# Optimization experiments

Measured on AMD Instinct MI355X. Metric: run time of the kernel, lower is better.

## Reference

```python
import jax, jax.numpy as jnp
import numpy as np

VOCAB = 4096
HIDDEN = 1024
BATCH = 64
SEQ = 256


def setup_inputs() -> dict:
    key = jax.random.key(0)
    ks = jax.random.split(key, 9)
    s = 0.02
    D = VOCAB + HIDDEN
    return {
        "X": jax.random.randint(ks[0], (BATCH, SEQ), 0, VOCAB),
        # gate weights stored as [in, out] = [VOCAB+HIDDEN, HIDDEN] (transposed torch Linear)
        "Wz": jax.random.normal(ks[1], (D, HIDDEN), dtype=jnp.float32) * s,
        "bz": jax.random.normal(ks[2], (HIDDEN,), dtype=jnp.float32) * s,
        "Wr": jax.random.normal(ks[3], (D, HIDDEN), dtype=jnp.float32) * s,
        "br": jax.random.normal(ks[4], (HIDDEN,), dtype=jnp.float32) * s,
        "Wh": jax.random.normal(ks[5], (D, HIDDEN), dtype=jnp.float32) * s,
        "bh": jax.random.normal(ks[6], (HIDDEN,), dtype=jnp.float32) * s,
        "Wo": jax.random.normal(ks[7], (HIDDEN, VOCAB), dtype=jnp.float32) * s,
        "bo": jax.random.normal(ks[8], (VOCAB,), dtype=jnp.float32) * s,
    }


def reference(X, Wz, bz, Wr, br, Wh, bh, Wo, bo):
    # X: [B, S] int tokens. torch does one_hot(X.T) -> time-major [S, B, V].
    # one_hot @ W_input_block == row gather of the input block of each gate weight.
    Xt = X.T  # [S, B]
    Wz_x, Wz_h = Wz[:VOCAB], Wz[VOCAB:]
    Wr_x, Wr_h = Wr[:VOCAB], Wr[VOCAB:]
    Wh_x, Wh_h = Wh[:VOCAB], Wh[VOCAB:]

    H0 = jnp.zeros((X.shape[0], HIDDEN), dtype=Wz.dtype)

    def step(H, x_t):
        # x_t: [B] int
        z = jax.nn.sigmoid(Wz_x[x_t] + H @ Wz_h + bz)
        r = jax.nn.sigmoid(Wr_x[x_t] + H @ Wr_h + br)
        h = jnp.tanh(Wh_x[x_t] + (r * H) @ Wh_h + bh)
        H_new = z * h + (1.0 - z) * H
        Y = H_new @ Wo + bo  # [B, V]
        return H_new, Y

    H_final, Ys = jax.lax.scan(step, H0, Xt)  # Ys: [S, B, V]
    # torch.cat(outputs, dim=0) over S tensors of [B, V] -> [S*B, V]
    out = Ys.reshape(-1, VOCAB)
    return out, (H_final,)
```

## Files before the change

### kernel.cpp

```cpp
#include <hip/hip_runtime.h>
#include <hip/hip_bf16.h>
#include <cstdint>
#include <cstddef>

#define VOCAB  4096
#define HIDDEN 1024
#define BATCH  64
#define SEQ    256
#define NWG    64

typedef __attribute__((ext_vector_type(8))) short short8;
typedef __attribute__((ext_vector_type(4))) float f32x4;
typedef unsigned long long u64;

__device__ __forceinline__ unsigned short f2bf(float f) {
    union { float f; uint32_t u; } v; v.f = f;
    uint32_t u = v.u;
    u += 0x7FFFu + ((u >> 16) & 1u);
    return (unsigned short)(u >> 16);
}

__device__ __forceinline__ void ast16(unsigned short* p, unsigned short v) {
    __hip_atomic_store(p, v, __ATOMIC_RELAXED, __HIP_MEMORY_SCOPE_AGENT);
}

__device__ __forceinline__ short8 cld16(const unsigned short* p) {
    short8 v;
    asm volatile("global_load_dwordx4 %0, %1, off sc0 sc1"
                 : "=v"(v) : "v"(p) : "memory");
    return v;
}

__global__ __launch_bounds__(256) void k_zero(float* Hf, unsigned short* Hbf, int* flags) {
    int i = blockIdx.x * 256 + threadIdx.x;
    if (i < BATCH * HIDDEN) { Hf[i] = 0.f; Hbf[i] = 0; }
    if (i < NWG * 32) flags[i] = 0;
}

__global__ __launch_bounds__(256) void k_pack(const float* __restrict__ src,
                                              unsigned short* __restrict__ dst,
                                              int R, int C) {
    __shared__ float tile[32][33];
    int tilesC = C >> 5;
    int bx = blockIdx.x % tilesC;
    int by = blockIdx.x / tilesC;
    int tx = threadIdx.x & 31;
    int ty = threadIdx.x >> 5;
    int c0 = bx << 5, r0 = by << 5;
    #pragma unroll
    for (int s = 0; s < 4; ++s) {
        int r = ty + s * 8;
        tile[r][tx] = src[(size_t)(r0 + r) * C + (c0 + tx)];
    }
    __syncthreads();
    #pragma unroll
    for (int s = 0; s < 4; ++s) {
        int cc = ty + s * 8;
        dst[(size_t)(c0 + cc) * R + (r0 + tx)] = f2bf(tile[tx][cc]);
    }
}

__device__ __forceinline__ void flag_barrier(int* flags, int p) {
    __syncthreads();
    if (threadIdx.x == 0)
        __hip_atomic_store(&flags[blockIdx.x * 32], p, __ATOMIC_RELEASE, __HIP_MEMORY_SCOPE_AGENT);
    if (threadIdx.x < NWG) {
        while (__hip_atomic_load(&flags[threadIdx.x * 32], __ATOMIC_RELAXED, __HIP_MEMORY_SCOPE_AGENT) < p)
            __builtin_amdgcn_s_sleep(1);
    }
    __syncthreads();
}

__global__ __launch_bounds__(256, 1) void k_scan(
    const int* __restrict__ X,
    const float* __restrict__ Wz, const float* __restrict__ bz,
    const float* __restrict__ Wr, const float* __restrict__ br,
    const float* __restrict__ Wh, const float* __restrict__ bh,
    const unsigned short* __restrict__ Wzh, const unsigned short* __restrict__ Wrh,
    const unsigned short* __restrict__ Whh,
    float* __restrict__ Hf, unsigned short* __restrict__ Hbf,
    unsigned short* __restrict__ rHbf, unsigned short* __restrict__ Hhist,
    int* __restrict__ flags)
{
    __shared__ __align__(16) unsigned short WzL[16 * 1024];
    __shared__ __align__(16) unsigned short WrL[16 * 1024];
    __shared__ __align__(16) unsigned short WhL[16 * 1024];

    const int tid  = threadIdx.x;
    const int g    = blockIdx.x;
    const int w    = tid >> 6;
    const int lane = tid & 63;
    const int row  = lane & 15;
    const int q    = lane >> 4;
    const int kq   = q << 3;
    const int col0 = g << 4;
    const int j    = col0 + row;
    const int b0   = w << 4;
    const int bq   = b0 + (q << 2);

    #pragma unroll
    for (int c = 0; c < 8; ++c) {
        int idx = tid + c * 256;
        int kkg = idx >> 6;
        int rem = idx & 63;
        int qq  = rem >> 4;
        int rr  = rem & 15;
        size_t srcoff = (size_t)(col0 + rr) * HIDDEN + kkg * 32 + qq * 8;
        *(short8*)&WzL[idx * 8] = *(const short8*)&Wzh[srcoff];
        *(short8*)&WrL[idx * 8] = *(const short8*)&Wrh[srcoff];
        *(short8*)&WhL[idx * 8] = *(const short8*)&Whh[srcoff];
    }
    __syncthreads();

    const float bzj = bz[j], brj = br[j], bhj = bh[j];

    float zreg[4] = {0.f, 0.f, 0.f, 0.f};
    float Hreg[4] = {0.f, 0.f, 0.f, 0.f};
    int p = 0;

    int   tok[4];
    float ez[4], er[4], eh[4];
    #pragma unroll
    for (int r = 0; r < 4; ++r) {
        tok[r] = X[(bq + r) * SEQ + 0];
        ez[r]  = Wz[(size_t)tok[r] * HIDDEN + j];
        er[r]  = Wr[(size_t)tok[r] * HIDDEN + j];
        eh[r]  = Wh[(size_t)tok[r] * HIDDEN + j];
    }

    for (int t = 0; t < SEQ; ++t) {
        {
            const unsigned short* ap = Hbf + (size_t)(b0 + row) * HIDDEN + kq;
            short8 A[32];
            #pragma unroll
            for (int kk = 0; kk < 32; ++kk)
                A[kk] = cld16(ap + kk * 32);

            f32x4 accZ = {0.f, 0.f, 0.f, 0.f}, accR = {0.f, 0.f, 0.f, 0.f};
            asm volatile("s_waitcnt vmcnt(16)" ::: "memory");
            __builtin_amdgcn_sched_barrier(0);
            #pragma unroll
            for (int kk = 0; kk < 16; ++kk) {
                short8 bzf = *(const short8*)&WzL[kk * 512 + q * 128 + row * 8];
                short8 brf = *(const short8*)&WrL[kk * 512 + q * 128 + row * 8];
                accZ = __builtin_amdgcn_mfma_f32_16x16x32_bf16(A[kk], bzf, accZ, 0, 0, 0);
                accR = __builtin_amdgcn_mfma_f32_16x16x32_bf16(A[kk], brf, accR, 0, 0, 0);
            }
            asm volatile("s_waitcnt vmcnt(0)" ::: "memory");
            __builtin_amdgcn_sched_barrier(0);
            #pragma unroll
            for (int kk = 16; kk < 32; ++kk) {
                short8 bzf = *(const short8*)&WzL[kk * 512 + q * 128 + row * 8];
                short8 brf = *(const short8*)&WrL[kk * 512 + q * 128 + row * 8];
                accZ = __builtin_amdgcn_mfma_f32_16x16x32_bf16(A[kk], bzf, accZ, 0, 0, 0);
                accR = __builtin_amdgcn_mfma_f32_16x16x32_bf16(A[kk], brf, accR, 0, 0, 0);
            }
            #pragma unroll
            for (int r = 0; r < 4; ++r) {
                float rr = 1.f / (1.f + expf(-(accR[r] + er[r] + brj)));
                ast16(&rHbf[(bq + r) * HIDDEN + j], f2bf(rr * Hreg[r]));
            }
            #pragma unroll
            for (int r = 0; r < 4; ++r)
                zreg[r] = 1.f / (1.f + expf(-(accZ[r] + ez[r] + bzj)));
        }

        flag_barrier(flags, ++p);

        {
            const unsigned short* ap = rHbf + (size_t)(b0 + row) * HIDDEN + kq;
            short8 A[32];
            #pragma unroll
            for (int kk = 0; kk < 32; ++kk)
                A[kk] = cld16(ap + kk * 32);

            f32x4 accA = {0.f, 0.f, 0.f, 0.f}, accB = {0.f, 0.f, 0.f, 0.f};
            asm volatile("s_waitcnt vmcnt(16)" ::: "memory");
            __builtin_amdgcn_sched_barrier(0);
            #pragma unroll
            for (int kk = 0; kk < 16; ++kk) {
                short8 bf = *(const short8*)&WhL[kk * 512 + q * 128 + row * 8];
                if (kk & 1) accB = __builtin_amdgcn_mfma_f32_16x16x32_bf16(A[kk], bf, accB, 0, 0, 0);
                else        accA = __builtin_amdgcn_mfma_f32_16x16x32_bf16(A[kk], bf, accA, 0, 0, 0);
            }
            asm volatile("s_waitcnt vmcnt(0)" ::: "memory");
            __builtin_amdgcn_sched_barrier(0);
            #pragma unroll
            for (int kk = 16; kk < 32; ++kk) {
                short8 bf = *(const short8*)&WhL[kk * 512 + q * 128 + row * 8];
                if (kk & 1) accB = __builtin_amdgcn_mfma_f32_16x16x32_bf16(A[kk], bf, accB, 0, 0, 0);
                else        accA = __builtin_amdgcn_mfma_f32_16x16x32_bf16(A[kk], bf, accA, 0, 0, 0);
            }
            #pragma unroll
            for (int r = 0; r < 4; ++r) {
                int b = bq + r;
                float h  = tanhf(accA[r] + accB[r] + eh[r] + bhj);
                float Hn = zreg[r] * h + (1.f - zreg[r]) * Hreg[r];
                Hreg[r] = Hn;
                unsigned short bfv = f2bf(Hn);
                ast16(&Hbf[b * HIDDEN + j], bfv);
                Hhist[(size_t)t * (BATCH * HIDDEN) + b * HIDDEN + j] = bfv;
                if (t == SEQ - 1) Hf[b * HIDDEN + j] = Hn;
            }
        }

        if (t + 1 < SEQ) {
            #pragma unroll
            for (int r = 0; r < 4; ++r) {
                tok[r] = X[(bq + r) * SEQ + (t + 1)];
                ez[r]  = Wz[(size_t)tok[r] * HIDDEN + j];
                er[r]  = Wr[(size_t)tok[r] * HIDDEN + j];
                eh[r]  = Wh[(size_t)tok[r] * HIDDEN + j];
            }
        }

        flag_barrier(flags, ++p);
    }
}

__global__ __launch_bounds__(256) void k_step1(
    const int* __restrict__ X,
    const float* __restrict__ Wz, const float* __restrict__ bz,
    const float* __restrict__ Wr, const float* __restrict__ br,
    const unsigned short* __restrict__ Wzh, const unsigned short* __restrict__ Wrh,
    const unsigned short* __restrict__ Hbf, const float* __restrict__ Hf,
    float* __restrict__ zbuf, unsigned short* __restrict__ rHbf, int t)
{
    int w    = threadIdx.x >> 6;
    int lane = threadIdx.x & 63;
    int nt = blockIdx.x;
    int mt = w;
    bool isz = nt < 64;
    const unsigned short* W = isz ? Wzh : Wrh;
    int ntl = nt & 63;
    int row = lane & 15;
    int kq  = (lane >> 4) << 3;
    const unsigned short* aptr = Hbf + (size_t)(mt * 16 + row) * HIDDEN + kq;
    const unsigned short* bptr = W   + (size_t)(ntl * 16 + row) * HIDDEN + kq;
    f32x4 acc = {0.f, 0.f, 0.f, 0.f};
    #pragma unroll 8
    for (int kk = 0; kk < HIDDEN / 32; ++kk) {
        short8 a = *(const short8*)(aptr + kk * 32);
        short8 b = *(const short8*)(bptr + kk * 32);
        acc = __builtin_amdgcn_mfma_f32_16x16x32_bf16(a, b, acc, 0, 0, 0);
    }
    int j = ntl * 16 + row;
    const float* Wemb = isz ? Wz : Wr;
    float bias = isz ? bz[j] : br[j];
    #pragma unroll
    for (int r = 0; r < 4; ++r) {
        int b = mt * 16 + ((lane >> 4) << 2) + r;
        int tok = X[b * SEQ + t];
        float pre = acc[r] + Wemb[(size_t)tok * HIDDEN + j] + bias;
        float s = 1.f / (1.f + expf(-pre));
        if (isz) zbuf[b * HIDDEN + j] = s;
        else     rHbf[b * HIDDEN + j] = f2bf(s * Hf[b * HIDDEN + j]);
    }
}

__global__ __launch_bounds__(256) void k_step2(
    const int* __restrict__ X,
    const float* __restrict__ Wh, const float* __restrict__ bh,
    const unsigned short* __restrict__ Whh,
    const unsigned short* __restrict__ rHbf,
    const float* __restrict__ zbuf,
    float* __restrict__ Hf, unsigned short* __restrict__ Hbf,
    unsigned short* __restrict__ Hhist, int t)
{
    int w    = threadIdx.x >> 6;
    int lane = threadIdx.x & 63;
    int nt = blockIdx.x;
    int mt = w;
    int row = lane & 15;
    int kq  = (lane >> 4) << 3;
    const unsigned short* aptr = rHbf + (size_t)(mt * 16 + row) * HIDDEN + kq;
    const unsigned short* bptr = Whh  + (size_t)(nt * 16 + row) * HIDDEN + kq;
    f32x4 acc = {0.f, 0.f, 0.f, 0.f};
    #pragma unroll 8
    for (int kk = 0; kk < HIDDEN / 32; ++kk) {
        short8 a = *(const short8*)(aptr + kk * 32);
        short8 b = *(const short8*)(bptr + kk * 32);
        acc = __builtin_amdgcn_mfma_f32_16x16x32_bf16(a, b, acc, 0, 0, 0);
    }
    int j = nt * 16 + row;
    float bias = bh[j];
    #pragma unroll
    for (int r = 0; r < 4; ++r) {
        int b = mt * 16 + ((lane >> 4) << 2) + r;
        int tok = X[b * SEQ + t];
        float pre = acc[r] + Wh[(size_t)tok * HIDDEN + j] + bias;
        float h = tanhf(pre);
        float z = zbuf[b * HIDDEN + j];
        float Hold = Hf[b * HIDDEN + j];
        float Hn = z * h + (1.f - z) * Hold;
        Hf[b * HIDDEN + j] = Hn;
        unsigned short bf = f2bf(Hn);
        Hbf[b * HIDDEN + j] = bf;
        Hhist[(size_t)t * (BATCH * HIDDEN) + b * HIDDEN + j] = bf;
    }
}

__global__ __launch_bounds__(256) void k_out(
    const unsigned short* __restrict__ A,
    const unsigned short* __restrict__ B,
    const float* __restrict__ bo,
    float* __restrict__ out)
{
    __shared__ __align__(16) unsigned short As[128 * 32];
    __shared__ __align__(16) unsigned short Bs[128 * 32];
    int bn = blockIdx.x & 31;
    int bm = blockIdx.x >> 5;
    int m0 = bm << 7, n0 = bn << 7;
    int tid  = threadIdx.x;
    int w    = tid >> 6, lane = tid & 63;
    int wm = w & 1, wn = w >> 1;
    int row = lane & 15;
    int kq  = (lane >> 4) << 3;

    f32x4 acc[4][4];
    #pragma unroll
    for (int i = 0; i < 4; ++i)
        #pragma unroll
        for (int jj = 0; jj < 4; ++jj)
            acc[i][jj] = (f32x4){0.f, 0.f, 0.f, 0.f};

    for (int k0 = 0; k0 < HIDDEN; k0 += 32) {
        #pragma unroll
        for (int c = 0; c < 2; ++c) {
            int off  = tid * 32 + c * 16;
            int rowi = off >> 6;
            int us   = (off & 63) >> 1;
            *(short8*)&As[rowi * 32 + us] =
                *(const short8*)&A[(size_t)(m0 + rowi) * HIDDEN + k0 + us];
            *(short8*)&Bs[rowi * 32 + us] =
                *(const short8*)&B[(size_t)(n0 + rowi) * HIDDEN + k0 + us];
        }
        __syncthreads();
        short8 a[4], b[4];
        #pragma unroll
        for (int i = 0; i < 4; ++i)
            a[i] = *(const short8*)&As[(wm * 64 + i * 16 + row) * 32 + kq];
        #pragma unroll
        for (int jj = 0; jj < 4; ++jj)
            b[jj] = *(const short8*)&Bs[(wn * 64 + jj * 16 + row) * 32 + kq];
        #pragma unroll
        for (int i = 0; i < 4; ++i)
            #pragma unroll
            for (int jj = 0; jj < 4; ++jj)
                acc[i][jj] = __builtin_amdgcn_mfma_f32_16x16x32_bf16(a[i], b[jj], acc[i][jj], 0, 0, 0);
        __syncthreads();
    }

    #pragma unroll
    for (int i = 0; i < 4; ++i) {
        #pragma unroll
        for (int jj = 0; jj < 4; ++jj) {
            int n = n0 + wn * 64 + jj * 16 + row;
            float bb = bo[n];
            #pragma unroll
            for (int r = 0; r < 4; ++r) {
                int m = m0 + wm * 64 + i * 16 + ((lane >> 4) << 2) + r;
                out[(size_t)m * VOCAB + n] = acc[i][jj][r] + bb;
            }
        }
    }
}

__global__ __launch_bounds__(256) void k_copyH(const float* __restrict__ Hf,
                                               float* __restrict__ out) {
    int i = blockIdx.x * 256 + threadIdx.x;
    if (i < BATCH * HIDDEN)
        out[(size_t)SEQ * BATCH * VOCAB + i] = Hf[i];
}

extern "C" void kernel_launch(void* const* d_in, const int* in_sizes, int n_in,
                              void* d_out, int out_size, void* d_ws, size_t ws_size,
                              hipStream_t stream) {
    const int*   X  = (const int*)  d_in[0];
    const float* Wz = (const float*)d_in[1];
    const float* bz = (const float*)d_in[2];
    const float* Wr = (const float*)d_in[3];
    const float* br = (const float*)d_in[4];
    const float* Wh = (const float*)d_in[5];
    const float* bh = (const float*)d_in[6];
    const float* Wo = (const float*)d_in[7];
    const float* bo = (const float*)d_in[8];
    float* out = (float*)d_out;
    char* ws = (char*)d_ws;

    float*          Hf    = (float*)(ws);
    float*          zbuf  = (float*)(ws + (256 << 10));
    int*            flags = (int*)(ws + (512 << 10));
    unsigned short* Hbf   = (unsigned short*)(ws + (528 << 10));
    unsigned short* rHbf  = (unsigned short*)(ws + (656 << 10));
    unsigned short* Wzh   = (unsigned short*)(ws + (1 << 20));
    unsigned short* Wrh   = Wzh + 1024 * 1024;
    unsigned short* Whh   = Wrh + 1024 * 1024;
    unsigned short* WoT   = Whh + 1024 * 1024;
    unsigned short* Hhist = WoT + (size_t)VOCAB * HIDDEN;

    k_zero<<<256, 256, 0, stream>>>(Hf, Hbf, flags);
    k_pack<<<32 * 32,  256, 0, stream>>>(Wz + (size_t)VOCAB * HIDDEN, Wzh, 1024, 1024);
    k_pack<<<32 * 32,  256, 0, stream>>>(Wr + (size_t)VOCAB * HIDDEN, Wrh, 1024, 1024);
    k_pack<<<32 * 32,  256, 0, stream>>>(Wh + (size_t)VOCAB * HIDDEN, Whh, 1024, 1024);
    k_pack<<<32 * 128, 256, 0, stream>>>(Wo, WoT, 1024, 4096);

    void* args[] = {
        (void*)&X, (void*)&Wz, (void*)&bz, (void*)&Wr, (void*)&br,
        (void*)&Wh, (void*)&bh, (void*)&Wzh, (void*)&Wrh, (void*)&Whh,
        (void*)&Hf, (void*)&Hbf, (void*)&rHbf, (void*)&Hhist, (void*)&flags
    };
    hipError_t cerr = hipLaunchCooperativeKernel((void*)k_scan, dim3(NWG), dim3(256),
                                                 args, 0, stream);
    if (cerr != hipSuccess) {
        for (int t = 0; t < SEQ; ++t) {
            k_step1<<<128, 256, 0, stream>>>(X, Wz, bz, Wr, br, Wzh, Wrh, Hbf, Hf, zbuf, rHbf, t);
            k_step2<<<64,  256, 0, stream>>>(X, Wh, bh, Whh, rHbf, zbuf, Hf, Hbf, Hhist, t);
        }
    }

    k_out<<<4096, 256, 0, stream>>>(Hhist, WoT, bo, out);
    k_copyH<<<256, 256, 0, stream>>>(Hf, out);
}
```

Before: 3.810 ms.

## Split scan into four independent batch groups with 16-workgroup barriers

Reorganizes the persistent scan kernel so each group of 16 workgroups handles 16 batch rows over all hidden columns, rather than every workgroup covering all 64 batch rows for 16 columns. The cross-workgroup barrier now synchronizes only the 16 workgroups of one group instead of all 64. The hidden-state tile is staged once per step into swizzled LDS, and the recurrent weights are streamed from global/L2 each step instead of being held resident in LDS. The intent is cheaper synchronization, at the cost of re-reading the weights every step and more global traffic.

```diff
diff --git a/kernel.cpp b/kernel.cpp
--- a/kernel.cpp
+++ b/kernel.cpp
@@ -8,10 +8,10 @@
 #define BATCH  64
 #define SEQ    256
 #define NWG    64
+#define SCANS  4
 
 typedef __attribute__((ext_vector_type(8))) short short8;
 typedef __attribute__((ext_vector_type(4))) float f32x4;
-typedef unsigned long long u64;
 
 __device__ __forceinline__ unsigned short f2bf(float f) {
     union { float f; uint32_t u; } v; v.f = f;
@@ -34,7 +34,7 @@
 __global__ __launch_bounds__(256) void k_zero(float* Hf, unsigned short* Hbf, int* flags) {
     int i = blockIdx.x * 256 + threadIdx.x;
     if (i < BATCH * HIDDEN) { Hf[i] = 0.f; Hbf[i] = 0; }
-    if (i < NWG * 32) flags[i] = 0;
+    if (i < 2048) flags[i] = 0;
 }
 
 __global__ __launch_bounds__(256) void k_pack(const float* __restrict__ src,
@@ -60,15 +60,18 @@
     }
 }
 
-__device__ __forceinline__ void flag_barrier(int* flags, int p) {
+__device__ __forceinline__ void grp_barrier(int* flags, int base, int idx, int p) {
+    asm volatile("s_waitcnt vmcnt(0)" ::: "memory");
     __syncthreads();
     if (threadIdx.x == 0)
-        __hip_atomic_store(&flags[blockIdx.x * 32], p, __ATOMIC_RELEASE, __HIP_MEMORY_SCOPE_AGENT);
-    if (threadIdx.x < NWG) {
-        while (__hip_atomic_load(&flags[threadIdx.x * 32], __ATOMIC_RELAXED, __HIP_MEMORY_SCOPE_AGENT) < p)
+        __hip_atomic_store(&flags[base + idx], p, __ATOMIC_RELAXED, __HIP_MEMORY_SCOPE_AGENT);
+    if (threadIdx.x < 16) {
+        while (__hip_atomic_load(&flags[base + (int)threadIdx.x],
+                                 __ATOMIC_RELAXED, __HIP_MEMORY_SCOPE_AGENT) < p)
             __builtin_amdgcn_s_sleep(1);
     }
     __syncthreads();
+    __builtin_amdgcn_sched_barrier(0);
 }
 
 __global__ __launch_bounds__(256, 1) void k_scan(
@@ -82,119 +85,124 @@
     unsigned short* __restrict__ rHbf, unsigned short* __restrict__ Hhist,
     int* __restrict__ flags)
 {
-    __shared__ __align__(16) unsigned short WzL[16 * 1024];
-    __shared__ __align__(16) unsigned short WrL[16 * 1024];
-    __shared__ __align__(16) unsigned short WhL[16 * 1024];
+    __shared__ __align__(16) unsigned short ALD[16 * 1024];
 
     const int tid  = threadIdx.x;
     const int g    = blockIdx.x;
-    const int w    = tid >> 6;
+    const int scan = g >> 4;
+    const int wgc  = g & 15;
+    const int wv   = tid >> 6;
     const int lane = tid & 63;
     const int row  = lane & 15;
     const int q    = lane >> 4;
     const int kq   = q << 3;
-    const int col0 = g << 4;
-    const int j    = col0 + row;
-    const int b0   = w << 4;
+    const int j    = (wgc << 6) + (wv << 4) + row;
+    const int b0   = scan << 4;
     const int bq   = b0 + (q << 2);
-
-    #pragma unroll
-    for (int c = 0; c < 8; ++c) {
-        int idx = tid + c * 256;
-        int kkg = idx >> 6;
-        int rem = idx & 63;
-        int qq  = rem >> 4;
-        int rr  = rem & 15;
-        size_t srcoff = (size_t)(col0 + rr) * HIDDEN + kkg * 32 + qq * 8;
-        *(short8*)&WzL[idx * 8] = *(const short8*)&Wzh[srcoff];
-        *(short8*)&WrL[idx * 8] = *(const short8*)&Wrh[srcoff];
-        *(short8*)&WhL[idx * 8] = *(const short8*)&Whh[srcoff];
-    }
-    __syncthreads();
+    const int fbase = scan << 4;
 
     const float bzj = bz[j], brj = br[j], bhj = bh[j];
+    const unsigned short* wzp = Wzh + (size_t)j * HIDDEN + kq;
+    const unsigned short* wrp = Wrh + (size_t)j * HIDDEN + kq;
+    const unsigned short* whp = Whh + (size_t)j * HIDDEN + kq;
 
     float zreg[4] = {0.f, 0.f, 0.f, 0.f};
     float Hreg[4] = {0.f, 0.f, 0.f, 0.f};
     int p = 0;
 
-    int   tok[4];
-    float ez[4], er[4], eh[4];
-    #pragma unroll
-    for (int r = 0; r < 4; ++r) {
-        tok[r] = X[(bq + r) * SEQ + 0];
-        ez[r]  = Wz[(size_t)tok[r] * HIDDEN + j];
-        er[r]  = Wr[(size_t)tok[r] * HIDDEN + j];
-        eh[r]  = Wh[(size_t)tok[r] * HIDDEN + j];
-    }
+    int tokc[4];
+    #pragma unroll
+    for (int r = 0; r < 4; ++r) tokc[r] = X[(bq + r) * SEQ + 0];
 
     for (int t = 0; t < SEQ; ++t) {
+        const int tn = (t + 1 < SEQ) ? t + 1 : t;
+        int tokn[4];
+
         {
-            const unsigned short* ap = Hbf + (size_t)(b0 + row) * HIDDEN + kq;
-            short8 A[32];
-            #pragma unroll
-            for (int kk = 0; kk < 32; ++kk)
-                A[kk] = cld16(ap + kk * 32);
+            {
+                short8 tmp[8];
+                #pragma unroll
+                for (int c = 0; c < 8; ++c) {
+                    int ch = (tid << 3) + c;
+                    int rw = ch >> 7;
+                    int k8 = ch & 127;
+                    tmp[c] = cld16(Hbf + (size_t)(b0 + rw) * HIDDEN + (k8 << 3));
+                }
+                asm volatile("s_waitcnt vmcnt(0)" ::: "memory");
+                __builtin_amdgcn_sched_barrier(0);
+                #pragma unroll
+                for (int c = 0; c < 8; ++c) {
+                    int ch = (tid << 3) + c;
+                    int rw = ch >> 7;
+                    int k8 = ch & 127;
+                    int ui = ((rw << 10) + (k8 << 3)) ^ ((rw & 7) << 3);
+                    *(short8*)&ALD[ui] = tmp[c];
+                }
+                __syncthreads();
+            }
+
+            float ez[4], er[4], eh[4];
+            #pragma unroll
+            for (int r = 0; r < 4; ++r) {
+                size_t eo = (size_t)tokc[r] * HIDDEN + j;
+                ez[r] = Wz[eo]; er[r] = Wr[eo]; eh[r] = Wh[eo];
+                tokn[r] = X[(bq + r) * SEQ + tn];
+            }
 
             f32x4 accZ = {0.f, 0.f, 0.f, 0.f}, accR = {0.f, 0.f, 0.f, 0.f};
-            asm volatile("s_waitcnt vmcnt(16)" ::: "memory");
-            __builtin_amdgcn_sched_barrier(0);
-            #pragma unroll
-            for (int kk = 0; kk < 16; ++kk) {
-                short8 bzf = *(const short8*)&WzL[kk * 512 + q * 128 + row * 8];
-                short8 brf = *(const short8*)&WrL[kk * 512 + q * 128 + row * 8];
-                accZ = __builtin_amdgcn_mfma_f32_16x16x32_bf16(A[kk], bzf, accZ, 0, 0, 0);
-                accR = __builtin_amdgcn_mfma_f32_16x16x32_bf16(A[kk], brf, accR, 0, 0, 0);
-            }
-            asm volatile("s_waitcnt vmcnt(0)" ::: "memory");
-            __builtin_amdgcn_sched_barrier(0);
-            #pragma unroll
-            for (int kk = 16; kk < 32; ++kk) {
-                short8 bzf = *(const short8*)&WzL[kk * 512 + q * 128 + row * 8];
-                short8 brf = *(const short8*)&WrL[kk * 512 + q * 128 + row * 8];
-                accZ = __builtin_amdgcn_mfma_f32_16x16x32_bf16(A[kk], bzf, accZ, 0, 0, 0);
-                accR = __builtin_amdgcn_mfma_f32_16x16x32_bf16(A[kk], brf, accR, 0, 0, 0);
+            #pragma unroll 8
+            for (int kk = 0; kk < 32; ++kk) {
+                int ai = ((row << 10) + (kk << 5) + kq) ^ ((row & 7) << 3);
+                short8 a  = *(const short8*)&ALD[ai];
+                short8 fz = *(const short8*)(wzp + kk * 32);
+                short8 fr = *(const short8*)(wrp + kk * 32);
+                accZ = __builtin_amdgcn_mfma_f32_16x16x32_bf16(a, fz, accZ, 0, 0, 0);
+                accR = __builtin_amdgcn_mfma_f32_16x16x32_bf16(a, fr, accR, 0, 0, 0);
             }
             #pragma unroll
             for (int r = 0; r < 4; ++r) {
-                float rr = 1.f / (1.f + expf(-(accR[r] + er[r] + brj)));
-                ast16(&rHbf[(bq + r) * HIDDEN + j], f2bf(rr * Hreg[r]));
-            }
-            #pragma unroll
-            for (int r = 0; r < 4; ++r)
+                float rv = 1.f / (1.f + expf(-(accR[r] + er[r] + brj)));
+                ast16(&rHbf[(bq + r) * HIDDEN + j], f2bf(rv * Hreg[r]));
                 zreg[r] = 1.f / (1.f + expf(-(accZ[r] + ez[r] + bzj)));
-        }
-
-        flag_barrier(flags, ++p);
-
-        {
-            const unsigned short* ap = rHbf + (size_t)(b0 + row) * HIDDEN + kq;
-            short8 A[32];
-            #pragma unroll
-            for (int kk = 0; kk < 32; ++kk)
-                A[kk] = cld16(ap + kk * 32);
-
-            f32x4 accA = {0.f, 0.f, 0.f, 0.f}, accB = {0.f, 0.f, 0.f, 0.f};
-            asm volatile("s_waitcnt vmcnt(16)" ::: "memory");
-            __builtin_amdgcn_sched_barrier(0);
-            #pragma unroll
-            for (int kk = 0; kk < 16; ++kk) {
-                short8 bf = *(const short8*)&WhL[kk * 512 + q * 128 + row * 8];
-                if (kk & 1) accB = __builtin_amdgcn_mfma_f32_16x16x32_bf16(A[kk], bf, accB, 0, 0, 0);
-                else        accA = __builtin_amdgcn_mfma_f32_16x16x32_bf16(A[kk], bf, accA, 0, 0, 0);
-            }
-            asm volatile("s_waitcnt vmcnt(0)" ::: "memory");
-            __builtin_amdgcn_sched_barrier(0);
-            #pragma unroll
-            for (int kk = 16; kk < 32; ++kk) {
-                short8 bf = *(const short8*)&WhL[kk * 512 + q * 128 + row * 8];
-                if (kk & 1) accB = __builtin_amdgcn_mfma_f32_16x16x32_bf16(A[kk], bf, accB, 0, 0, 0);
-                else        accA = __builtin_amdgcn_mfma_f32_16x16x32_bf16(A[kk], bf, accA, 0, 0, 0);
+            }
+            #pragma unroll
+            for (int r = 0; r < 4; ++r) zreg[r] = zreg[r];
+            grp_barrier(flags, fbase, wgc, ++p);
+
+            {
+                short8 tmp[8];
+                #pragma unroll
+                for (int c = 0; c < 8; ++c) {
+                    int ch = (tid << 3) + c;
+                    int rw = ch >> 7;
+                    int k8 = ch & 127;
+                    tmp[c] = cld16(rHbf + (size_t)(b0 + rw) * HIDDEN + (k8 << 3));
+                }
+                asm volatile("s_waitcnt vmcnt(0)" ::: "memory");
+                __builtin_amdgcn_sched_barrier(0);
+                #pragma unroll
+                for (int c = 0; c < 8; ++c) {
+                    int ch = (tid << 3) + c;
+                    int rw = ch >> 7;
+                    int k8 = ch & 127;
+                    int ui = ((rw << 10) + (k8 << 3)) ^ ((rw & 7) << 3);
+                    *(short8*)&ALD[ui] = tmp[c];
+                }
+                __syncthreads();
+            }
+
+            f32x4 accH = {0.f, 0.f, 0.f, 0.f};
+            #pragma unroll 8
+            for (int kk = 0; kk < 32; ++kk) {
+                int ai = ((row << 10) + (kk << 5) + kq) ^ ((row & 7) << 3);
+                short8 a  = *(const short8*)&ALD[ai];
+                short8 fh = *(const short8*)(whp + kk * 32);
+                accH = __builtin_amdgcn_mfma_f32_16x16x32_bf16(a, fh, accH, 0, 0, 0);
             }
             #pragma unroll
             for (int r = 0; r < 4; ++r) {
                 int b = bq + r;
-                float h  = tanhf(accA[r] + accB[r] + eh[r] + bhj);
+                float h  = tanhf(accH[r] + eh[r] + bhj);
                 float Hn = zreg[r] * h + (1.f - zreg[r]) * Hreg[r];
                 Hreg[r] = Hn;
                 unsigned short bfv = f2bf(Hn);
@@ -202,19 +210,11 @@
                 Hhist[(size_t)t * (BATCH * HIDDEN) + b * HIDDEN + j] = bfv;
                 if (t == SEQ - 1) Hf[b * HIDDEN + j] = Hn;
             }
+            grp_barrier(flags, fbase, wgc, ++p);
         }
 
-        if (t + 1 < SEQ) {
-            #pragma unroll
-            for (int r = 0; r < 4; ++r) {
-                tok[r] = X[(bq + r) * SEQ + (t + 1)];
-                ez[r]  = Wz[(size_t)tok[r] * HIDDEN + j];
-                er[r]  = Wr[(size_t)tok[r] * HIDDEN + j];
-                eh[r]  = Wh[(size_t)tok[r] * HIDDEN + j];
-            }
-        }
-
-        flag_barrier(flags, ++p);
+        #pragma unroll
+        for (int r = 0; r < 4; ++r) tokc[r] = tokn[r];
     }
 }
 
```

After: 5.170 ms. +35.7%, slower.
